# Performance work log

Measured on AMD Instinct MI355X. Metric: run time of the kernel, lower is better.

Reference implementation:

```python
import jax, jax.numpy as jnp
import numpy as np

D_MODEL = 1024
N_EXPERTS = 8
TOP_K = 2
LN_EPS = 1e-5


def setup_inputs() -> dict:
    key = jax.random.key(0)
    ks = jax.random.split(key, 8)
    B, S, d, E = 2, 2048, D_MODEL, N_EXPERTS
    f = 2 * d
    s_in = 0.02
    return {
        "x": jax.random.normal(ks[0], (B, S, d), jnp.float32),
        "Wg": jax.random.normal(ks[1], (d, E), jnp.float32) * s_in,
        "bg": jnp.zeros((E,), jnp.float32),
        "W1": jax.random.normal(ks[2], (E, d, f), jnp.float32) * s_in,
        "b1": jnp.zeros((E, f), jnp.float32),
        "W2": jax.random.normal(ks[3], (E, f, d), jnp.float32) * s_in,
        "b2": jnp.zeros((E, d), jnp.float32),
        "gamma": jnp.ones((d,), jnp.float32),
        "beta": jnp.zeros((d,), jnp.float32),
    }


def reference(x, Wg, bg, W1, b1, W2, b2, gamma, beta):
    # Gating + top-k routing (softmax over the selected top-k logits only)
    logits = jnp.einsum("bsd,de->bse", x, Wg) + bg            # [B,S,E]
    topk_vals, topk_idx = jax.lax.top_k(logits, TOP_K)         # [B,S,K]
    topk_w = jax.nn.softmax(topk_vals, axis=-1)                # [B,S,K]

    # Expert MLPs evaluated densely for all experts (dropout is identity in eval)
    h = jax.nn.relu(jnp.einsum("bsd,edf->bsef", x, W1) + b1)   # [B,S,E,2d]
    eo = jnp.einsum("bsef,efd->bsed", h, W2) + b2              # [B,S,E,d]

    # Gather the top-k experts' outputs per token and combine with gate weights
    sel = jnp.take_along_axis(eo, topk_idx[..., None], axis=2)  # [B,S,K,d]
    mixed = jnp.sum(sel * topk_w[..., None], axis=2)            # [B,S,d]

    # Residual + LayerNorm
    y = mixed + x
    mu = jnp.mean(y, axis=-1, keepdims=True)
    var = jnp.mean(jnp.square(y - mu), axis=-1, keepdims=True)
    return gamma * (y - mu) * jax.lax.rsqrt(var + LN_EPS) + beta
```

## Files before the change

kernel.cpp:

```cpp
#include <hip/hip_runtime.h>


typedef unsigned short ushort_t;
typedef short short8 __attribute__((ext_vector_type(8)));
typedef float f32x4 __attribute__((ext_vector_type(4)));

#define T_TOKENS 4096
#define DMODEL 1024
#define FFN 2048
#define NEXP 8
#define MAXSLOTS 9216
#define GATE_BLOCKS 1024
#define TOK_PER_BLK 4
#define MAX_MT 12

__device__ __forceinline__ ushort_t f2bf(float f) {
    unsigned u = __float_as_uint(f);
    return (ushort_t)((u + 0x7fffu + ((u >> 16) & 1u)) >> 16);
}
__device__ __forceinline__ float bflo(unsigned packed) {
    return __uint_as_float(packed << 16);
}
__device__ __forceinline__ float bfhi(unsigned packed) {
    return __uint_as_float(packed & 0xffff0000u);
}

__device__ __forceinline__ void gload_lds16(const void* g, void* l) {
    __builtin_amdgcn_global_load_lds(
        (const __attribute__((address_space(1))) unsigned int*)g,
        (__attribute__((address_space(3))) unsigned int*)l,
        16, 0, 0);
}

__global__ __launch_bounds__(256) void gate_kernel(
    const float* __restrict__ x, const float* __restrict__ Wg,
    const float* __restrict__ bg,
    int* __restrict__ top_idx, float* __restrict__ top_w,
    int* __restrict__ blk_hist)
{
    __shared__ int hist[NEXP];
    const int tid = threadIdx.x, lane = tid & 63, w = tid >> 6;
    if (tid < NEXP) hist[tid] = 0;
    __syncthreads();

    const int t = blockIdx.x * TOK_PER_BLK + w;
    const float* xr = x + (size_t)t * DMODEL;
    float acc[8] = {0.f,0.f,0.f,0.f,0.f,0.f,0.f,0.f};
    #pragma unroll
    for (int i = 0; i < 16; i++) {
        float xv = xr[i * 64 + lane];
        const float4* wp = (const float4*)&Wg[(i * 64 + lane) * 8];
        float4 a = wp[0], b = wp[1];
        acc[0] += xv * a.x; acc[1] += xv * a.y;
        acc[2] += xv * a.z; acc[3] += xv * a.w;
        acc[4] += xv * b.x; acc[5] += xv * b.y;
        acc[6] += xv * b.z; acc[7] += xv * b.w;
    }
    #pragma unroll
    for (int off = 32; off > 0; off >>= 1) {
        #pragma unroll
        for (int e = 0; e < 8; e++) acc[e] += __shfl_down(acc[e], off);
    }
    if (lane == 0) {
        float l[8];
        #pragma unroll
        for (int e = 0; e < 8; e++) l[e] = acc[e] + bg[e];
        int i0 = 0; float v0 = l[0];
        #pragma unroll
        for (int e = 1; e < 8; e++) if (l[e] > v0) { v0 = l[e]; i0 = e; }
        int i1 = -1; float v1 = -1e30f;
        #pragma unroll
        for (int e = 0; e < 8; e++) if (e != i0 && l[e] > v1) { v1 = l[e]; i1 = e; }
        float eg = expf(v1 - v0);
        float den = 1.f + eg;
        int p0 = atomicAdd(&hist[i0], 1);
        int p1 = atomicAdd(&hist[i1], 1);
        top_idx[2 * t]     = i0 | (p0 << 4);
        top_idx[2 * t + 1] = i1 | (p1 << 4);
        top_w[2 * t]     = 1.f / den;
        top_w[2 * t + 1] = eg / den;
    }
    __syncthreads();
    if (tid < NEXP) blk_hist[blockIdx.x * NEXP + tid] = hist[tid];
}

__global__ __launch_bounds__(512) void scan_kernel(
    const int* __restrict__ blk_hist, int* __restrict__ blk_base,
    int* __restrict__ offs)
{
    __shared__ int cnt[NEXP];
    const int tid = threadIdx.x, lane = tid & 63, e = tid >> 6;
    int orig[GATE_BLOCKS / 64];
    #pragma unroll
    for (int r = 0; r < GATE_BLOCKS / 64; r++)
        orig[r] = blk_hist[(r * 64 + lane) * NEXP + e];
    int carry = 0;
    #pragma unroll
    for (int r = 0; r < GATE_BLOCKS / 64; r++) {
        int v = orig[r];
        #pragma unroll
        for (int off = 1; off < 64; off <<= 1) {
            int u = __shfl_up(v, off);
            if (lane >= off) v += u;
        }
        blk_base[(r * 64 + lane) * NEXP + e] = carry + v - orig[r];
        carry += __shfl(v, 63);
    }
    if (lane == 0) cnt[e] = carry;
    __syncthreads();
    if (tid == 0) {
        int cum = 0;
        for (int ee = 0; ee < NEXP; ee++) {
            offs[ee] = cum;
            cum += (cnt[ee] + 127) & ~127;
        }
        offs[NEXP] = cum;
    }
}

__global__ __launch_bounds__(256) void scatter_gather_kernel(
    const float* __restrict__ x, const int* __restrict__ top_idx,
    const int* __restrict__ offs, const int* __restrict__ blk_base,
    int* __restrict__ slot_of, ushort_t* __restrict__ Xg)
{
    const int t = blockIdx.x, tid = threadIdx.x;
    __shared__ int slots[2];
    if (tid < 2) {
        int v = top_idx[2 * t + tid];
        int e = v & 15, pos = v >> 4;
        int gb = t / TOK_PER_BLK;
        int slot = offs[e] + blk_base[gb * NEXP + e] + pos;
        slot_of[2 * t + tid] = slot;
        slots[tid] = slot;
    }
    __syncthreads();
    float4 xv = ((const float4*)(x + (size_t)t * DMODEL))[tid];
    uint2 pk;
    pk.x = f2bf(xv.x) | ((unsigned)f2bf(xv.y) << 16);
    pk.y = f2bf(xv.z) | ((unsigned)f2bf(xv.w) << 16);
    ((uint2*)(Xg + (size_t)slots[0] * DMODEL))[tid] = pk;
    ((uint2*)(Xg + (size_t)slots[1] * DMODEL))[tid] = pk;
}

__global__ __launch_bounds__(256) void transpose_kernel(
    const float* __restrict__ W1, const float* __restrict__ W2,
    ushort_t* __restrict__ W1T, ushort_t* __restrict__ W2T)
{
    int b = blockIdx.x;
    const float* s; ushort_t* d; int N, kc, ns;
    if (b < 1024) {
        int e = b >> 7, idx = b & 127;
        kc = idx >> 2; ns = idx & 3;
        s = W1 + (size_t)e * DMODEL * FFN;
        d = W1T + (size_t)e * DMODEL * FFN;
        N = FFN;
    } else {
        b -= 1024;
        int e = b >> 7, idx = b & 127;
        kc = idx >> 1; ns = idx & 1;
        s = W2 + (size_t)e * DMODEL * FFN;
        d = W2T + (size_t)e * DMODEL * FFN;
        N = DMODEL;
    }
    const int k0 = kc * 32, n0 = ns * 512;
    const int tid = threadIdx.x;

    __shared__ __align__(16) ushort_t lt[32][516];

    #pragma unroll
    for (int i = 0; i < 16; i++) {
        int k = i * 2 + (tid >> 7);
        int n = (tid & 127) * 4;
        float4 v = *(const float4*)&s[(size_t)(k0 + k) * N + n0 + n];
        uint2 pk;
        pk.x = (unsigned)f2bf(v.x) | ((unsigned)f2bf(v.y) << 16);
        pk.y = (unsigned)f2bf(v.z) | ((unsigned)f2bf(v.w) << 16);
        *(uint2*)&lt[k][n] = pk;
    }
    __syncthreads();

    {
        const int sub = tid & 3;
        const int nl0 = tid >> 2;
        #pragma unroll
        for (int it = 0; it < 8; it++) {
            int n = nl0 + it * 64;
            uint4 o;
            o.x = (unsigned)lt[sub * 8 + 0][n] | ((unsigned)lt[sub * 8 + 1][n] << 16);
            o.y = (unsigned)lt[sub * 8 + 2][n] | ((unsigned)lt[sub * 8 + 3][n] << 16);
            o.z = (unsigned)lt[sub * 8 + 4][n] | ((unsigned)lt[sub * 8 + 5][n] << 16);
            o.w = (unsigned)lt[sub * 8 + 6][n] | ((unsigned)lt[sub * 8 + 7][n] << 16);
            *(uint4*)&d[((size_t)kc * N + n0 + n) * 32 + sub * 8] = o;
        }
    }
}

template <int K, int N, bool RELU>
__global__ __launch_bounds__(256) void expert_gemm(
    const ushort_t* __restrict__ A,
    const ushort_t* __restrict__ Bt,
    const float* __restrict__ bias,
    ushort_t* __restrict__ Cout,
    const int* __restrict__ offs)
{
    const int e  = blockIdx.x;
    const int nt = blockIdx.y;
    const int mt = blockIdx.z;
    const int off_e = offs[e];
    const int Mpad  = offs[e + 1] - off_e;
    if (mt * 128 >= Mpad) return;

    __shared__ __align__(16) ushort_t As[128 * 32];
    __shared__ __align__(16) ushort_t Bs[128 * 32];

    const int tid  = threadIdx.x;
    const int lane = tid & 63;
    const int w    = tid >> 6;
    const int quad = lane >> 4;
    const int r16  = lane & 15;
    const int lrow = lane >> 2;
    const int lk   = (((lane & 3) ^ ((lane >> 3) & 3))) * 8;

    const size_t arow0 = (size_t)(off_e + mt * 128);
    const ushort_t* aS0 = A + (arow0 + (size_t)(2 * w + 0) * 16 + lrow) * K + lk;
    const ushort_t* aS1 = A + (arow0 + (size_t)(2 * w + 1) * 16 + lrow) * K + lk;
    const ushort_t* Bte = Bt + (size_t)e * N * K;
    const ushort_t* bS0 = Bte + (size_t)(nt * 128 + (2 * w + 0) * 16 + lrow) * 32 + lk;
    const ushort_t* bS1 = Bte + (size_t)(nt * 128 + (2 * w + 1) * 16 + lrow) * 32 + lk;
    ushort_t* aD0 = &As[(2 * w + 0) * 512];
    ushort_t* aD1 = &As[(2 * w + 1) * 512];
    ushort_t* bD0 = &Bs[(2 * w + 0) * 512];
    ushort_t* bD1 = &Bs[(2 * w + 1) * 512];

    const int wm = (w >> 1) * 64;
    const int wn = (w & 1) * 64;
    const int sw = ((r16 >> 1) & 3) ^ quad;

    f32x4 acc[4][4];
    #pragma unroll
    for (int i = 0; i < 4; i++)
        #pragma unroll
        for (int j = 0; j < 4; j++)
            acc[i][j] = (f32x4){0.f, 0.f, 0.f, 0.f};

    for (int k0 = 0; k0 < K; k0 += 32) {
        gload_lds16(aS0 + k0, aD0);
        gload_lds16(aS1 + k0, aD1);
        gload_lds16(bS0 + (size_t)k0 * N, bD0);
        gload_lds16(bS1 + (size_t)k0 * N, bD1);
        __syncthreads();
        short8 af[4], bfr[4];
        #pragma unroll
        for (int i = 0; i < 4; i++)
            af[i] = *(const short8*)&As[(wm + i * 16 + r16) * 32 + sw * 8];
        #pragma unroll
        for (int j = 0; j < 4; j++)
            bfr[j] = *(const short8*)&Bs[(wn + j * 16 + r16) * 32 + sw * 8];
        #pragma unroll
        for (int i = 0; i < 4; i++)
            #pragma unroll
            for (int j = 0; j < 4; j++)
                acc[i][j] = __builtin_amdgcn_mfma_f32_16x16x32_bf16(
                    af[i], bfr[j], acc[i][j], 0, 0, 0);
        __syncthreads();
    }

    const float* be = bias + (size_t)e * N;
    #pragma unroll
    for (int i = 0; i < 4; i++) {
        #pragma unroll
        for (int j = 0; j < 4; j++) {
            int n = nt * 128 + wn + j * 16 + r16;
            float bv = be[n];
            #pragma unroll
            for (int r = 0; r < 4; r++) {
                int m = mt * 128 + wm + i * 16 + quad * 4 + r;
                float v = acc[i][j][r] + bv;
                if (RELU) v = v > 0.f ? v : 0.f;
                Cout[(size_t)(off_e + m) * N + n] = f2bf(v);
            }
        }
    }
}

__global__ __launch_bounds__(256) void ln_kernel(
    const float* __restrict__ x, const ushort_t* __restrict__ O,
    const int* __restrict__ slot_of, const float* __restrict__ top_w,
    const float* __restrict__ gamma, const float* __restrict__ beta,
    float* __restrict__ out)
{
    int t = blockIdx.x, tid = threadIdx.x;
    int s0 = slot_of[2 * t], s1 = slot_of[2 * t + 1];
    float w0 = top_w[2 * t], w1 = top_w[2 * t + 1];
    float4 xv = ((const float4*)(x + (size_t)t * DMODEL))[tid];
    uint2 a = ((const uint2*)(O + (size_t)s0 * DMODEL))[tid];
    uint2 b = ((const uint2*)(O + (size_t)s1 * DMODEL))[tid];

    float y[4];
    y[0] = xv.x + w0 * bflo(a.x) + w1 * bflo(b.x);
    y[1] = xv.y + w0 * bfhi(a.x) + w1 * bfhi(b.x);
    y[2] = xv.z + w0 * bflo(a.y) + w1 * bflo(b.y);
    y[3] = xv.w + w0 * bfhi(a.y) + w1 * bfhi(b.y);

    float s = y[0] + y[1] + y[2] + y[3];
    float sq = y[0]*y[0] + y[1]*y[1] + y[2]*y[2] + y[3]*y[3];
    __shared__ float red[2][4];
    #pragma unroll
    for (int off = 32; off > 0; off >>= 1) {
        s += __shfl_down(s, off);
        sq += __shfl_down(sq, off);
    }
    int lane = tid & 63, wv = tid >> 6;
    if (lane == 0) { red[0][wv] = s; red[1][wv] = sq; }
    __syncthreads();
    if (tid == 0) {
        float S = red[0][0] + red[0][1] + red[0][2] + red[0][3];
        float SQ = red[1][0] + red[1][1] + red[1][2] + red[1][3];
        float mu = S * (1.f / DMODEL);
        float var = SQ * (1.f / DMODEL) - mu * mu;
        red[0][0] = mu;
        red[1][0] = rsqrtf(var + 1e-5f);
    }
    __syncthreads();
    float mu = red[0][0], inv = red[1][0];
    float4 gv = ((const float4*)gamma)[tid];
    float4 bv = ((const float4*)beta)[tid];
    float4 ov;
    ov.x = gv.x * (y[0] - mu) * inv + bv.x;
    ov.y = gv.y * (y[1] - mu) * inv + bv.y;
    ov.z = gv.z * (y[2] - mu) * inv + bv.z;
    ov.w = gv.w * (y[3] - mu) * inv + bv.w;
    ((float4*)(out + (size_t)t * DMODEL))[tid] = ov;
}

extern "C" void kernel_launch(void* const* d_in, const int* in_sizes, int n_in,
                              void* d_out, int out_size, void* d_ws, size_t ws_size,
                              hipStream_t stream)
{
    const float* x     = (const float*)d_in[0];
    const float* Wg    = (const float*)d_in[1];
    const float* bg    = (const float*)d_in[2];
    const float* W1    = (const float*)d_in[3];
    const float* b1    = (const float*)d_in[4];
    const float* W2    = (const float*)d_in[5];
    const float* b2    = (const float*)d_in[6];
    const float* gamma = (const float*)d_in[7];
    const float* beta  = (const float*)d_in[8];
    float* out = (float*)d_out;

    char* ws = (char*)d_ws;
    size_t o = 0;
    auto alloc = [&](size_t bytes) {
        size_t r = o;
        o = (o + bytes + 255) & ~(size_t)255;
        return r;
    };
    size_t o_offs    = alloc((NEXP + 1) * 4);
    size_t o_topidx  = alloc((size_t)T_TOKENS * 2 * 4);
    size_t o_topw    = alloc((size_t)T_TOKENS * 2 * 4);
    size_t o_slotof  = alloc((size_t)T_TOKENS * 2 * 4);
    size_t o_bhist   = alloc((size_t)GATE_BLOCKS * NEXP * 4);
    size_t o_bbase   = alloc((size_t)GATE_BLOCKS * NEXP * 4);
    size_t o_w1t     = alloc((size_t)NEXP * DMODEL * FFN * 2);
    size_t o_w2t     = alloc((size_t)NEXP * DMODEL * FFN * 2);
    size_t o_xg      = alloc((size_t)MAXSLOTS * DMODEL * 2);
    size_t o_h       = alloc((size_t)MAXSLOTS * FFN * 2);
    size_t o_obuf    = alloc((size_t)MAXSLOTS * DMODEL * 2);
    (void)ws_size; (void)in_sizes; (void)n_in; (void)out_size;

    int*      offs     = (int*)(ws + o_offs);
    int*      top_idx  = (int*)(ws + o_topidx);
    float*    top_w    = (float*)(ws + o_topw);
    int*      slot_of  = (int*)(ws + o_slotof);
    int*      blk_hist = (int*)(ws + o_bhist);
    int*      blk_base = (int*)(ws + o_bbase);
    ushort_t* W1T      = (ushort_t*)(ws + o_w1t);
    ushort_t* W2T      = (ushort_t*)(ws + o_w2t);
    ushort_t* Xg       = (ushort_t*)(ws + o_xg);
    ushort_t* H        = (ushort_t*)(ws + o_h);
    ushort_t* Obuf     = (ushort_t*)(ws + o_obuf);

    gate_kernel<<<GATE_BLOCKS, 256, 0, stream>>>(x, Wg, bg, top_idx, top_w, blk_hist);
    transpose_kernel<<<2048, 256, 0, stream>>>(W1, W2, W1T, W2T);
    scan_kernel<<<1, 512, 0, stream>>>(blk_hist, blk_base, offs);
    scatter_gather_kernel<<<T_TOKENS, 256, 0, stream>>>(x, top_idx, offs, blk_base, slot_of, Xg);
    expert_gemm<DMODEL, FFN, true>
        <<<dim3(NEXP, FFN / 128, MAX_MT), 256, 0, stream>>>(Xg, W1T, b1, H, offs);
    expert_gemm<FFN, DMODEL, false>
        <<<dim3(NEXP, DMODEL / 128, MAX_MT), 256, 0, stream>>>(H, W2T, b2, Obuf, offs);
    ln_kernel<<<T_TOKENS, 256, 0, stream>>>(x, Obuf, slot_of, top_w, gamma, beta, out);
}
```

Measured before the change: 319.9 us.

## Fuse gating, scatter and weight transpose; use fixed per-expert capacity slots

Replaces the gate, scan and scatter kernels with a single prep kernel. Each token now gets its slot directly from global atomics into a fixed-capacity per-expert region (ECAP rows per expert), and the same kernel packs x to bf16 into those slots. The W1 transpose runs in extra blocks of the prep kernel, and the W2 transpose is folded into spare z-blocks of the first expert GEMM, so conversion work overlaps with routing and compute and several launches and the prefix scan go away. The cost is that per-expert capacity is capped at 1152 rows, down from up to 1536, which relies on routing staying close to balanced. Global atomic ordering also makes slot assignment nondeterministic.

```diff
diff --git a/kernel.cpp b/kernel.cpp
--- a/kernel.cpp
+++ b/kernel.cpp
@@ -9,10 +9,9 @@
 #define DMODEL 1024
 #define FFN 2048
 #define NEXP 8
+#define ECAP 1152
 #define MAXSLOTS 9216
-#define GATE_BLOCKS 1024
-#define TOK_PER_BLK 4
-#define MAX_MT 12
+#define MT1 9
 
 __device__ __forceinline__ ushort_t f2bf(float f) {
     unsigned u = __float_as_uint(f);
@@ -32,186 +31,135 @@
         16, 0, 0);
 }
 
-__global__ __launch_bounds__(256) void gate_kernel(
-    const float* __restrict__ x, const float* __restrict__ Wg,
-    const float* __restrict__ bg,
-    int* __restrict__ top_idx, float* __restrict__ top_w,
-    int* __restrict__ blk_hist)
-{
-    __shared__ int hist[NEXP];
-    const int tid = threadIdx.x, lane = tid & 63, w = tid >> 6;
-    if (tid < NEXP) hist[tid] = 0;
-    __syncthreads();
-
-    const int t = blockIdx.x * TOK_PER_BLK + w;
-    const float* xr = x + (size_t)t * DMODEL;
-    float acc[8] = {0.f,0.f,0.f,0.f,0.f,0.f,0.f,0.f};
-    #pragma unroll
-    for (int i = 0; i < 16; i++) {
-        float xv = xr[i * 64 + lane];
-        const float4* wp = (const float4*)&Wg[(i * 64 + lane) * 8];
-        float4 a = wp[0], b = wp[1];
-        acc[0] += xv * a.x; acc[1] += xv * a.y;
-        acc[2] += xv * a.z; acc[3] += xv * a.w;
-        acc[4] += xv * b.x; acc[5] += xv * b.y;
-        acc[6] += xv * b.z; acc[7] += xv * b.w;
-    }
-    #pragma unroll
-    for (int off = 32; off > 0; off >>= 1) {
-        #pragma unroll
-        for (int e = 0; e < 8; e++) acc[e] += __shfl_down(acc[e], off);
-    }
-    if (lane == 0) {
-        float l[8];
-        #pragma unroll
-        for (int e = 0; e < 8; e++) l[e] = acc[e] + bg[e];
-        int i0 = 0; float v0 = l[0];
-        #pragma unroll
-        for (int e = 1; e < 8; e++) if (l[e] > v0) { v0 = l[e]; i0 = e; }
-        int i1 = -1; float v1 = -1e30f;
-        #pragma unroll
-        for (int e = 0; e < 8; e++) if (e != i0 && l[e] > v1) { v1 = l[e]; i1 = e; }
-        float eg = expf(v1 - v0);
-        float den = 1.f + eg;
-        int p0 = atomicAdd(&hist[i0], 1);
-        int p1 = atomicAdd(&hist[i1], 1);
-        top_idx[2 * t]     = i0 | (p0 << 4);
-        top_idx[2 * t + 1] = i1 | (p1 << 4);
-        top_w[2 * t]     = 1.f / den;
-        top_w[2 * t + 1] = eg / den;
-    }
-    __syncthreads();
-    if (tid < NEXP) blk_hist[blockIdx.x * NEXP + tid] = hist[tid];
-}
-
-__global__ __launch_bounds__(512) void scan_kernel(
-    const int* __restrict__ blk_hist, int* __restrict__ blk_base,
-    int* __restrict__ offs)
-{
-    __shared__ int cnt[NEXP];
-    const int tid = threadIdx.x, lane = tid & 63, e = tid >> 6;
-    int orig[GATE_BLOCKS / 64];
-    #pragma unroll
-    for (int r = 0; r < GATE_BLOCKS / 64; r++)
-        orig[r] = blk_hist[(r * 64 + lane) * NEXP + e];
-    int carry = 0;
-    #pragma unroll
-    for (int r = 0; r < GATE_BLOCKS / 64; r++) {
-        int v = orig[r];
-        #pragma unroll
-        for (int off = 1; off < 64; off <<= 1) {
-            int u = __shfl_up(v, off);
-            if (lane >= off) v += u;
-        }
-        blk_base[(r * 64 + lane) * NEXP + e] = carry + v - orig[r];
-        carry += __shfl(v, 63);
-    }
-    if (lane == 0) cnt[e] = carry;
-    __syncthreads();
-    if (tid == 0) {
-        int cum = 0;
-        for (int ee = 0; ee < NEXP; ee++) {
-            offs[ee] = cum;
-            cum += (cnt[ee] + 127) & ~127;
-        }
-        offs[NEXP] = cum;
-    }
-}
-
-__global__ __launch_bounds__(256) void scatter_gather_kernel(
-    const float* __restrict__ x, const int* __restrict__ top_idx,
-    const int* __restrict__ offs, const int* __restrict__ blk_base,
-    int* __restrict__ slot_of, ushort_t* __restrict__ Xg)
-{
-    const int t = blockIdx.x, tid = threadIdx.x;
-    __shared__ int slots[2];
-    if (tid < 2) {
-        int v = top_idx[2 * t + tid];
-        int e = v & 15, pos = v >> 4;
-        int gb = t / TOK_PER_BLK;
-        int slot = offs[e] + blk_base[gb * NEXP + e] + pos;
-        slot_of[2 * t + tid] = slot;
-        slots[tid] = slot;
-    }
-    __syncthreads();
-    float4 xv = ((const float4*)(x + (size_t)t * DMODEL))[tid];
-    uint2 pk;
-    pk.x = f2bf(xv.x) | ((unsigned)f2bf(xv.y) << 16);
-    pk.y = f2bf(xv.z) | ((unsigned)f2bf(xv.w) << 16);
-    ((uint2*)(Xg + (size_t)slots[0] * DMODEL))[tid] = pk;
-    ((uint2*)(Xg + (size_t)slots[1] * DMODEL))[tid] = pk;
-}
-
-__global__ __launch_bounds__(256) void transpose_kernel(
-    const float* __restrict__ W1, const float* __restrict__ W2,
-    ushort_t* __restrict__ W1T, ushort_t* __restrict__ W2T)
-{
-    int b = blockIdx.x;
-    const float* s; ushort_t* d; int N, kc, ns;
-    if (b < 1024) {
-        int e = b >> 7, idx = b & 127;
-        kc = idx >> 2; ns = idx & 3;
-        s = W1 + (size_t)e * DMODEL * FFN;
-        d = W1T + (size_t)e * DMODEL * FFN;
-        N = FFN;
-    } else {
-        b -= 1024;
-        int e = b >> 7, idx = b & 127;
-        kc = idx >> 1; ns = idx & 1;
-        s = W2 + (size_t)e * DMODEL * FFN;
-        d = W2T + (size_t)e * DMODEL * FFN;
-        N = DMODEL;
-    }
-    const int k0 = kc * 32, n0 = ns * 512;
+__device__ __forceinline__ void wt_block(
+    const float* __restrict__ Wsrc, ushort_t* __restrict__ Wdst,
+    int e, int kc, int ns, int N, ushort_t* sm)
+{
+    const float* s = Wsrc + (size_t)e * DMODEL * FFN;
+    ushort_t* d = Wdst + (size_t)e * DMODEL * FFN;
+    const int k0 = kc * 32, n0 = ns * 256;
     const int tid = threadIdx.x;
-
-    __shared__ __align__(16) ushort_t lt[32][516];
-
-    #pragma unroll
-    for (int i = 0; i < 16; i++) {
-        int k = i * 2 + (tid >> 7);
-        int n = (tid & 127) * 4;
+    #pragma unroll
+    for (int i = 0; i < 8; i++) {
+        int k = i * 4 + (tid >> 6);
+        int n = (tid & 63) * 4;
         float4 v = *(const float4*)&s[(size_t)(k0 + k) * N + n0 + n];
         uint2 pk;
         pk.x = (unsigned)f2bf(v.x) | ((unsigned)f2bf(v.y) << 16);
         pk.y = (unsigned)f2bf(v.z) | ((unsigned)f2bf(v.w) << 16);
-        *(uint2*)&lt[k][n] = pk;
+        *(uint2*)&sm[k * 260 + n] = pk;
     }
     __syncthreads();
-
-    {
-        const int sub = tid & 3;
-        const int nl0 = tid >> 2;
-        #pragma unroll
-        for (int it = 0; it < 8; it++) {
-            int n = nl0 + it * 64;
-            uint4 o;
-            o.x = (unsigned)lt[sub * 8 + 0][n] | ((unsigned)lt[sub * 8 + 1][n] << 16);
-            o.y = (unsigned)lt[sub * 8 + 2][n] | ((unsigned)lt[sub * 8 + 3][n] << 16);
-            o.z = (unsigned)lt[sub * 8 + 4][n] | ((unsigned)lt[sub * 8 + 5][n] << 16);
-            o.w = (unsigned)lt[sub * 8 + 6][n] | ((unsigned)lt[sub * 8 + 7][n] << 16);
-            *(uint4*)&d[((size_t)kc * N + n0 + n) * 32 + sub * 8] = o;
-        }
-    }
-}
-
-template <int K, int N, bool RELU>
+    const int sub = tid & 3;
+    const int nl0 = tid >> 2;
+    #pragma unroll
+    for (int it = 0; it < 4; it++) {
+        int n = nl0 + it * 64;
+        uint4 o;
+        o.x = (unsigned)sm[(sub * 8 + 0) * 260 + n] | ((unsigned)sm[(sub * 8 + 1) * 260 + n] << 16);
+        o.y = (unsigned)sm[(sub * 8 + 2) * 260 + n] | ((unsigned)sm[(sub * 8 + 3) * 260 + n] << 16);
+        o.z = (unsigned)sm[(sub * 8 + 4) * 260 + n] | ((unsigned)sm[(sub * 8 + 5) * 260 + n] << 16);
+        o.w = (unsigned)sm[(sub * 8 + 6) * 260 + n] | ((unsigned)sm[(sub * 8 + 7) * 260 + n] << 16);
+        *(uint4*)&d[((size_t)kc * N + n0 + n) * 32 + sub * 8] = o;
+    }
+}
+
+__global__ __launch_bounds__(256) void prep_kernel(
+    const float* __restrict__ W1, ushort_t* __restrict__ W1T,
+    const float* __restrict__ x, const float* __restrict__ Wg,
+    const float* __restrict__ bg,
+    int* __restrict__ cnt, int* __restrict__ slot_of,
+    float* __restrict__ top_w, ushort_t* __restrict__ Xg)
+{
+    __shared__ __align__(16) ushort_t smem[32 * 260];
+    const int b = blockIdx.x;
+    const int tid = threadIdx.x;
+    if (b < 2048) {
+        int e = b >> 8, idx = b & 255;
+        wt_block(W1, W1T, e, idx >> 3, idx & 7, FFN, smem);
+        return;
+    }
+    const int g = b - 2048;
+    const int lane = tid & 63, w = tid >> 6;
+    const int t = g * 4 + w;
+    const float* xr = x + (size_t)t * DMODEL;
+    float acc[8] = {0.f,0.f,0.f,0.f,0.f,0.f,0.f,0.f};
+    #pragma unroll
+    for (int i = 0; i < 16; i++) {
+        float xv = xr[i * 64 + lane];
+        const float4* wp = (const float4*)&Wg[(i * 64 + lane) * 8];
+        float4 a = wp[0], bb = wp[1];
+        acc[0] += xv * a.x;  acc[1] += xv * a.y;
+        acc[2] += xv * a.z;  acc[3] += xv * a.w;
+        acc[4] += xv * bb.x; acc[5] += xv * bb.y;
+        acc[6] += xv * bb.z; acc[7] += xv * bb.w;
+    }
+    #pragma unroll
+    for (int off = 32; off > 0; off >>= 1) {
+        #pragma unroll
+        for (int e = 0; e < 8; e++) acc[e] += __shfl_down(acc[e], off);
+    }
+    int s0, s1;
+    if (lane == 0) {
+        float l[8];
+        #pragma unroll
+        for (int e = 0; e < 8; e++) l[e] = acc[e] + bg[e];
+        int i0 = 0; float v0 = l[0];
+        #pragma unroll
+        for (int e = 1; e < 8; e++) if (l[e] > v0) { v0 = l[e]; i0 = e; }
+        int i1 = -1; float v1 = -1e30f;
+        #pragma unroll
+        for (int e = 0; e < 8; e++) if (e != i0 && l[e] > v1) { v1 = l[e]; i1 = e; }
+        float eg = expf(v1 - v0);
+        float den = 1.f + eg;
+        int p0 = atomicAdd(&cnt[i0], 1);
+        int p1 = atomicAdd(&cnt[i1], 1);
+        s0 = i0 * ECAP + p0;
+        s1 = i1 * ECAP + p1;
+        slot_of[2 * t]     = s0;
+        slot_of[2 * t + 1] = s1;
+        top_w[2 * t]     = 1.f / den;
+        top_w[2 * t + 1] = eg / den;
+    }
+    s0 = __shfl(s0, 0);
+    s1 = __shfl(s1, 0);
+    #pragma unroll
+    for (int j = 0; j < 4; j++) {
+        int f = lane + j * 64;
+        float4 xv = ((const float4*)xr)[f];
+        uint2 pk;
+        pk.x = (unsigned)f2bf(xv.x) | ((unsigned)f2bf(xv.y) << 16);
+        pk.y = (unsigned)f2bf(xv.z) | ((unsigned)f2bf(xv.w) << 16);
+        ((uint2*)(Xg + (size_t)s0 * DMODEL))[f] = pk;
+        ((uint2*)(Xg + (size_t)s1 * DMODEL))[f] = pk;
+    }
+}
+
+template <int K, int N, bool RELU, bool FUSET>
 __global__ __launch_bounds__(256) void expert_gemm(
     const ushort_t* __restrict__ A,
     const ushort_t* __restrict__ Bt,
     const float* __restrict__ bias,
     ushort_t* __restrict__ Cout,
-    const int* __restrict__ offs)
-{
+    const int* __restrict__ cnt,
+    const float* __restrict__ Wsrc,
+    ushort_t* __restrict__ Wdst)
+{
+    __shared__ __align__(16) ushort_t smem[32 * 260];
+    if (FUSET && blockIdx.z >= MT1) {
+        int idx = (blockIdx.z - MT1) * 128 + blockIdx.y * 8 + blockIdx.x;
+        int e = idx >> 8, r = idx & 255;
+        wt_block(Wsrc, Wdst, e, r >> 2, r & 3, DMODEL, smem);
+        return;
+    }
     const int e  = blockIdx.x;
     const int nt = blockIdx.y;
     const int mt = blockIdx.z;
-    const int off_e = offs[e];
-    const int Mpad  = offs[e + 1] - off_e;
-    if (mt * 128 >= Mpad) return;
-
-    __shared__ __align__(16) ushort_t As[128 * 32];
-    __shared__ __align__(16) ushort_t Bs[128 * 32];
+    const int off_e = e * ECAP;
+    if (mt * 128 >= cnt[e]) return;
+
+    ushort_t* As = smem;
+    ushort_t* Bs = smem + 4096;
 
     const int tid  = threadIdx.x;
     const int lane = tid & 63;
@@ -355,12 +303,9 @@
         o = (o + bytes + 255) & ~(size_t)255;
         return r;
     };
-    size_t o_offs    = alloc((NEXP + 1) * 4);
-    size_t o_topidx  = alloc((size_t)T_TOKENS * 2 * 4);
+    size_t o_cnt     = alloc(NEXP * 4);
     size_t o_topw    = alloc((size_t)T_TOKENS * 2 * 4);
     size_t o_slotof  = alloc((size_t)T_TOKENS * 2 * 4);
-    size_t o_bhist   = alloc((size_t)GATE_BLOCKS * NEXP * 4);
-    size_t o_bbase   = alloc((size_t)GATE_BLOCKS * NEXP * 4);
     size_t o_w1t     = alloc((size_t)NEXP * DMODEL * FFN * 2);
     size_t o_w2t     = alloc((size_t)NEXP * DMODEL * FFN * 2);
     size_t o_xg      = alloc((size_t)MAXSLOTS * DMODEL * 2);
@@ -368,25 +313,23 @@
     size_t o_obuf    = alloc((size_t)MAXSLOTS * DMODEL * 2);
     (void)ws_size; (void)in_sizes; (void)n_in; (void)out_size;
 
-    int*      offs     = (int*)(ws + o_offs);
-    int*      top_idx  = (int*)(ws + o_topidx);
+    int*      cnt      = (int*)(ws + o_cnt);
     float*    top_w    = (float*)(ws + o_topw);
     int*      slot_of  = (int*)(ws + o_slotof);
-    int*      blk_hist = (int*)(ws + o_bhist);
-    int*      blk_base = (int*)(ws + o_bbase);
     ushort_t* W1T      = (ushort_t*)(ws + o_w1t);
     ushort_t* W2T      = (ushort_t*)(ws + o_w2t);
     ushort_t* Xg       = (ushort_t*)(ws + o_xg);
     ushort_t* H        = (ushort_t*)(ws + o_h);
     ushort_t* Obuf     = (ushort_t*)(ws + o_obuf);
 
-    gate_kernel<<<GATE_BLOCKS, 256, 0, stream>>>(x, Wg, bg, top_idx, top_w, blk_hist);
-    transpose_kernel<<<2048, 256, 0, stream>>>(W1, W2, W1T, W2T);
-    scan_kernel<<<1, 512, 0, stream>>>(blk_hist, blk_base, offs);
-    scatter_gather_kernel<<<T_TOKENS, 256, 0, stream>>>(x, top_idx, offs, blk_base, slot_of, Xg);
-    expert_gemm<DMODEL, FFN, true>
-        <<<dim3(NEXP, FFN / 128, MAX_MT), 256, 0, stream>>>(Xg, W1T, b1, H, offs);
-    expert_gemm<FFN, DMODEL, false>
-        <<<dim3(NEXP, DMODEL / 128, MAX_MT), 256, 0, stream>>>(H, W2T, b2, Obuf, offs);
+    hipMemsetAsync(cnt, 0, NEXP * sizeof(int), stream);
+    prep_kernel<<<3072, 256, 0, stream>>>(W1, W1T, x, Wg, bg,
+                                          cnt, slot_of, top_w, Xg);
+    expert_gemm<DMODEL, FFN, true, true>
+        <<<dim3(NEXP, FFN / 128, MT1 + 16), 256, 0, stream>>>(
+            Xg, W1T, b1, H, cnt, W2, W2T);
+    expert_gemm<FFN, DMODEL, false, false>
+        <<<dim3(NEXP, DMODEL / 128, MT1), 256, 0, stream>>>(
+            H, W2T, b2, Obuf, cnt, nullptr, nullptr);
     ln_kernel<<<T_TOKENS, 256, 0, stream>>>(x, Obuf, slot_of, top_w, gamma, beta, out);
 }
```

New measurement: 376.6 us. 17.7% more time.
